# Optimization experiments

Measured on AMD Instinct MI355X. Metric: run time of the kernel, lower is better.

The kernel has to match this reference:

```python
import jax, jax.numpy as jnp
import numpy as np

SR = 44100
N_FFT = 2048
N_BINS = 64
HOP = 512
POWER = 2.0
FREQ_BINS = N_FFT // 2 + 1  # 1025
BATCH = 32
LEN_AUDIO = 441000  # 10 seconds at 44.1 kHz


def _fourier_kernels():
    # Periodic (fftbins=True) Hann window, matching scipy.signal.get_window('hann', n_fft)
    n = np.arange(N_FFT)
    window = 0.5 - 0.5 * np.cos(2.0 * np.pi * n / N_FFT)
    k = np.arange(FREQ_BINS)[:, None]  # [freq_bins, 1]
    phase = 2.0 * np.pi * k * n[None, :] / N_FFT  # [freq_bins, n_fft]
    wsin = (np.sin(phase) * window[None, :]).astype(np.float32)[:, None, :]  # [F,1,n_fft]
    wcos = (np.cos(phase) * window[None, :]).astype(np.float32)[:, None, :]
    return jnp.asarray(wsin), jnp.asarray(wcos)


def setup_inputs() -> dict:
    key = jax.random.key(0)
    k1, k2 = jax.random.split(key)
    x = jax.random.normal(k1, (BATCH, 1, LEN_AUDIO), dtype=jnp.float32)
    wsin, wcos = _fourier_kernels()
    # Gammatone filterbank matrix [n_bins, freq_bins]; treated as a fixed parameter.
    gammatone_basis = jax.random.uniform(k2, (N_BINS, FREQ_BINS), dtype=jnp.float32) * 0.01
    return {"x": x, "wsin": wsin, "wcos": wcos, "gammatone_basis": gammatone_basis}


def _conv1d(x, w, stride):
    # x: [B, 1, L], w: [F, 1, K] -> [B, F, T]
    return jax.lax.conv_general_dilated(
        x, w, window_strides=(stride,), padding='VALID',
        dimension_numbers=('NCH', 'OIH', 'NCH'))


def reference(x, wsin, wcos, gammatone_basis):
    pad = N_FFT // 2
    xp = jnp.pad(x, ((0, 0), (0, 0), (pad, pad)), mode='reflect')
    s = _conv1d(xp, wsin, HOP)
    c = _conv1d(xp, wcos, HOP)
    spec = jnp.sqrt(s * s + c * c) ** POWER  # [B, F, T]
    # [n_bins, F] @ [B, F, T] -> [B, n_bins, T]
    return jnp.einsum('nf,bft->bnt', gammatone_basis, spec)
```

## Files before the change

kernel.cpp:

```cpp
#include <hip/hip_runtime.h>
#include <stdint.h>

typedef __attribute__((ext_vector_type(4))) float f32x4;
typedef __attribute__((ext_vector_type(8))) short bf16x8;
typedef __attribute__((ext_vector_type(8))) unsigned short u16x8;
typedef __attribute__((ext_vector_type(2))) unsigned int u32x2;

#define B_SZ   32
#define L_AUD  441000
#define PAD_A  1024
#define LP     443048
#define T_FR   862
#define J_TOT  27584
#define JPAD   27648
#define F_BINS 1025
#define NFFT   2048
#define NB     64
#define FPAD   1152
#define NT_J   108
#define NT_F   9
#define NWG    (NT_J * NT_F)
#define ROWB   886096

#define W2_OFF     0
#define W2_BYTES   (NT_F * 32 * 16384)
#define GB2_OFF    W2_BYTES
#define GB2_BYTES  (NB * FPAD * 2)
#define UB_OFF     (GB2_OFF + GB2_BYTES)
#define UB_BYTES   ((size_t)JPAD * 2048 * 2)
#define WS_FOLD    (UB_OFF + UB_BYTES)
#define SLAB_BYTES ((size_t)NT_F * NB * JPAD * 4)
#define WS_FOLD_SLAB (WS_FOLD + SLAB_BYTES)

#define FB_XBP_OFF   0
#define FB_XBP_BYTES (B_SZ * LP * 2)
#define FB_WBT_OFF   FB_XBP_BYTES
#define FB_WBT_BYTES (NT_F * 32 * 2 * 16384)
#define FB_GB_OFF    (FB_WBT_OFF + FB_WBT_BYTES)
#define FB_WS_NEED   (FB_GB_OFF + GB2_BYTES)
#define FB_SLAB_OFF  FB_WS_NEED
#define FB_WS_BIG    ((size_t)FB_SLAB_OFF + SLAB_BYTES)

__device__ __forceinline__ uint16_t f2bf(float f) {
  union { float f; uint32_t u; } c; c.f = f;
  uint32_t r = c.u + 0x7FFFu + ((c.u >> 16) & 1u);
  return (uint16_t)(r >> 16);
}

__device__ __forceinline__ f32x4 mfma16(bf16x8 a, bf16x8 b, f32x4 c) {
  return __builtin_amdgcn_mfma_f32_16x16x32_bf16(a, b, c, 0, 0, 0);
}

#define GLD16(g, l) __builtin_amdgcn_global_load_lds( \
    (__attribute__((address_space(1))) void*)(g),     \
    (__attribute__((address_space(3))) void*)(l), 16, 0, 0)

__device__ __forceinline__ int refl(int p) {
  int s = p - PAD_A;
  s = s < 0 ? -s : s;
  s = s >= L_AUD ? (2 * L_AUD - 2 - s) : s;
  return s;
}


__global__ __launch_bounds__(256) void build_gb(const float* __restrict__ g,
                                                uint16_t* __restrict__ gb) {
  int i = blockIdx.x * 256 + threadIdx.x;
  int n = i / FPAD;
  int f = i - n * FPAD;
  gb[i] = f2bf(f < F_BINS ? g[n * F_BINS + f] : 0.0f);
}

__global__ __launch_bounds__(256) void reduce9(const float* __restrict__ slab,
                                               float* __restrict__ out) {
  int i = blockIdx.x * 256 + threadIdx.x;
  if (i >= J_TOT * NB) return;
  int b = i / (NB * T_FR);
  int rem = i - b * (NB * T_FR);
  int n = rem / T_FR;
  int t = rem - n * T_FR;
  int j = b * T_FR + t;
  float s = 0.f;
#pragma unroll
  for (int fb = 0; fb < NT_F; ++fb)
    s += slab[((size_t)fb * NB + n) * JPAD + j];
  out[i] = s;
}


__global__ __launch_bounds__(256) void build_wbt2(const float* __restrict__ wsin,
                                                  const float* __restrict__ wcos,
                                                  uint16_t* __restrict__ wbt) {
  int idx = blockIdx.x * 256 + threadIdx.x;
  int e = idx & 7;
  int s = (idx >> 3) & 7;
  int jp = (idx >> 6) & 127;
  int kkt = (idx >> 13) & 31;
  int fb = idx >> 18;
  int v = s ^ (jp & 7);
  int r = jp * 2 + (v >> 2);
  int k = (v & 3) * 8 + e;
  int plane = r >> 7;
  int f = fb * 128 + (r & 127);
  int m = kkt * 32 + k;
  float val = 0.f;
  if (f < F_BINS) {
    int mm = (m == 0) ? 1024 : m;
    val = plane ? wsin[(size_t)f * NFFT + mm] : wcos[(size_t)f * NFFT + mm];
  }
  wbt[idx] = f2bf(val);
}

__global__ __launch_bounds__(128) void build_ub(const float* __restrict__ x,
                                                uint16_t* __restrict__ ub) {
  __shared__ float xs[2048];
  int jg = blockIdx.x;
  int tid = threadIdx.x;
  uint16_t* outp = ub + (size_t)jg * 2048;
  if (jg >= J_TOT) {
    u16x8 z = (u16x8)0;
    *(u16x8*)(outp + tid * 8) = z;
    *(u16x8*)(outp + 1024 + tid * 8) = z;
    return;
  }
  int b = jg / T_FR, t = jg - b * T_FR;
  int c = t * 512;
  const float* xb = x + (size_t)b * L_AUD;
  if (t >= 2 && t <= 859) {
    const float4* src = (const float4*)(xb + c - PAD_A);
    float4* dl = (float4*)xs;
#pragma unroll
    for (int i = 0; i < 4; ++i) dl[tid * 4 + i] = src[tid * 4 + i];
  } else {
#pragma unroll
    for (int i = 0; i < 16; ++i) xs[tid * 16 + i] = xb[refl(c + tid * 16 + i)];
  }
  __syncthreads();
  int m0 = tid * 8;
  u16x8 vp, vm;
#pragma unroll
  for (int i = 0; i < 8; ++i) {
    int m = m0 + i;
    if (m == 0) { vp[i] = f2bf(xs[1024]); vm[i] = 0; }
    else {
      float a = xs[m], r = xs[2048 - m];
      vp[i] = f2bf(a + r);
      vm[i] = f2bf(a - r);
    }
  }
  *(u16x8*)(outp + m0) = vp;
  *(u16x8*)(outp + 1024 + m0) = vm;
}

template <bool USE_SLAB>
__global__ __launch_bounds__(512, 2) void gammatone_fold(
    const char* __restrict__ ub, const char* __restrict__ wbt2,
    const char* __restrict__ gb, float* __restrict__ dst) {
  __shared__ __align__(16) char smem[147456];

  const int tid = threadIdx.x;
  const int w = tid >> 6, l = tid & 63;
  const int lgrp = l >> 4, l15 = l & 15;
  const int fh = w >> 2, jq = w & 3;

  const int orig = blockIdx.x;
  const int xcd = orig & 7, slot = orig >> 3;
  const int q = NWG / 8, r = NWG & 7;
  const int wkid = (xcd < r ? xcd * (q + 1) : r * (q + 1) + (xcd - r) * q) + slot;
  const int jb = wkid / NT_F;
  const int fb = wkid - jb * NT_F;
  const int j0 = jb * 256;
  const int f0 = fb * 128;

  const int ssn = w >> 2, q4 = w & 3;
  const int aoff_sta = w * 2048 + l * 16;
  const int boff_sta = 16384 + ssn * 16384 + q4 * 4096 + l * 16;
  const int vsw = (l & 7) ^ (l >> 3);
  const char* bsrc[4];
#pragma unroll
  for (int i = 0; i < 4; ++i) {
    int col = j0 + q4 * 64 + i * 16 + (l >> 3) * 2 + (vsw >> 2);
    bsrc[i] = ub + (size_t)col * 4096 + ssn * 2048 + (vsw & 3) * 16;
  }
  const char* wbtA = wbt2 + (size_t)fb * 524288;

#define STAGEF(kkt, off) do {                                               \
    const char* ga_ = wbtA + (size_t)(kkt) * 16384 + aoff_sta;              \
    GLD16(ga_,        smem + (off) + aoff_sta);                             \
    GLD16(ga_ + 1024, smem + (off) + aoff_sta + 1024);                      \
    GLD16(bsrc[0] + (size_t)(kkt) * 64, smem + (off) + boff_sta);           \
    GLD16(bsrc[1] + (size_t)(kkt) * 64, smem + (off) + boff_sta + 1024);    \
    GLD16(bsrc[2] + (size_t)(kkt) * 64, smem + (off) + boff_sta + 2048);    \
    GLD16(bsrc[3] + (size_t)(kkt) * 64, smem + (off) + boff_sta + 3072);    \
  } while (0)

  const int slb = ((lgrp | ((l15 & 1) << 2)) ^ (l15 >> 1)) << 4;
  int aoff[8], bpo[4], bmo[4];
#pragma unroll
  for (int m = 0; m < 8; ++m)
    aoff[m] = ((m >> 2) * 64 + fh * 32 + (m & 3) * 8 + (l15 >> 1)) * 128 + slb;
#pragma unroll
  for (int n = 0; n < 4; ++n) {
    bpo[n] = 16384 + (jq * 32 + n * 8 + (l15 >> 1)) * 128 + slb;
    bmo[n] = bpo[n] + 16384;
  }

  STAGEF(0, 0);
  STAGEF(1, 49152);
  asm volatile("s_waitcnt vmcnt(6)" ::: "memory");
  asm volatile("s_barrier" ::: "memory");

  f32x4 acc[8][4];
#pragma unroll
  for (int m = 0; m < 8; ++m)
#pragma unroll
    for (int n = 0; n < 4; ++n) acc[m][n] = (f32x4){0.f, 0.f, 0.f, 0.f};

  unsigned b0 = 0, b1 = 49152, b2 = 98304;
  for (int kk = 0; kk < 32; ++kk) {
    bf16x8 av[8], bp[4], bm[4];
#pragma unroll
    for (int m = 0; m < 8; ++m) av[m] = *(const bf16x8*)(smem + b0 + aoff[m]);
#pragma unroll
    for (int n = 0; n < 4; ++n) {
      bp[n] = *(const bf16x8*)(smem + b0 + bpo[n]);
      bm[n] = *(const bf16x8*)(smem + b0 + bmo[n]);
    }
    if (kk < 30) STAGEF(kk + 2, b2);
    __builtin_amdgcn_s_setprio(1);
#pragma unroll
    for (int m = 0; m < 4; ++m)
#pragma unroll
      for (int n = 0; n < 4; ++n) {
        acc[m][n]     = mfma16(av[m],     bp[n], acc[m][n]);
        acc[m + 4][n] = mfma16(av[m + 4], bm[n], acc[m + 4][n]);
      }
    __builtin_amdgcn_s_setprio(0);
    if (kk < 30)       asm volatile("s_waitcnt vmcnt(6)" ::: "memory");
    else if (kk == 30) asm volatile("s_waitcnt vmcnt(0)" ::: "memory");
    asm volatile("s_barrier" ::: "memory");
    unsigned t = b0; b0 = b1; b1 = b2; b2 = t;
  }

#pragma unroll
  for (int m = 0; m < 4; ++m) {
    int fi = fh * 64 + m * 16 + lgrp * 4;
#pragma unroll
    for (int n = 0; n < 4; ++n) {
      int j = jq * 64 + n * 16 + l15;
      f32x4 c = acc[m][n], s = acc[m + 4][n];
      uint32_t lo = (uint32_t)f2bf(s.x * s.x + c.x * c.x) |
                    ((uint32_t)f2bf(s.y * s.y + c.y * c.y) << 16);
      uint32_t hi = (uint32_t)f2bf(s.z * s.z + c.z * c.z) |
                    ((uint32_t)f2bf(s.w * s.w + c.w * c.w) << 16);
      int off = j * 256 + ((fi * 2) ^ ((j & 7) << 4));
      *(u32x2*)(smem + off) = (u32x2){lo, hi};
    }
  }
  __syncthreads();

  f32x4 acc2[4][2];
#pragma unroll
  for (int m = 0; m < 4; ++m) {
    acc2[m][0] = (f32x4){0.f, 0.f, 0.f, 0.f};
    acc2[m][1] = (f32x4){0.f, 0.f, 0.f, 0.f};
  }
  const int jw = w * 32;
#pragma unroll
  for (int ks = 0; ks < 4; ++ks) {
    bf16x8 gf[4], sf[2];
#pragma unroll
    for (int m2 = 0; m2 < 4; ++m2) {
      int grow = m2 * 16 + l15;
      gf[m2] = *(const bf16x8*)(gb + ((size_t)grow * FPAD + f0 + ks * 32 + lgrp * 8) * 2);
    }
#pragma unroll
    for (int nf = 0; nf < 2; ++nf) {
      int j = jw + nf * 16 + l15;
      sf[nf] = *(const bf16x8*)(smem + j * 256 + (((ks * 32 + lgrp * 8) * 2) ^ ((j & 7) << 4)));
    }
#pragma unroll
    for (int m2 = 0; m2 < 4; ++m2)
#pragma unroll
      for (int nf = 0; nf < 2; ++nf)
        acc2[m2][nf] = mfma16(gf[m2], sf[nf], acc2[m2][nf]);
  }

#pragma unroll
  for (int nf = 0; nf < 2; ++nf) {
    int jg = j0 + jw + nf * 16 + l15;
    if (USE_SLAB) {
      float* sl = dst + ((size_t)fb * NB) * JPAD + jg;
#pragma unroll
      for (int m2 = 0; m2 < 4; ++m2)
#pragma unroll
        for (int r2 = 0; r2 < 4; ++r2) {
          int nout = m2 * 16 + lgrp * 4 + r2;
          sl[(size_t)nout * JPAD] = acc2[m2][nf][r2];
        }
    } else if (jg < J_TOT) {
      int b = jg / T_FR;
      int t = jg - b * T_FR;
      float* ob = dst + (size_t)(b * NB) * T_FR + t;
#pragma unroll
      for (int m2 = 0; m2 < 4; ++m2)
#pragma unroll
        for (int r2 = 0; r2 < 4; ++r2) {
          int nout = m2 * 16 + lgrp * 4 + r2;
          atomicAdd(ob + (size_t)nout * T_FR, acc2[m2][nf][r2]);
        }
    }
  }
}


__global__ __launch_bounds__(256) void build_xbp(const float* __restrict__ x,
                                                 uint16_t* __restrict__ xbp) {
  int i = blockIdx.x * 256 + threadIdx.x;
  int b = i / LP;
  int p = i - b * LP;
  xbp[i] = f2bf(x[b * L_AUD + refl(p)]);
}

__global__ __launch_bounds__(256) void build_wbtf(const float* __restrict__ wsin,
                                                  const float* __restrict__ wcos,
                                                  uint16_t* __restrict__ wbt) {
  int idx = blockIdx.x * 256 + threadIdx.x;
  int e = idx & 7;
  int l = (idx >> 3) & 63;
  int s = (idx >> 9) & 1;
  int fm = (idx >> 10) & 15;
  int kkt = (idx >> 14) & 31;
  int fb = idx >> 19;
  int tr = fm * 16 + (l & 15);
  int k = kkt * 64 + s * 32 + ((l >> 4) << 3) + e;
  int plane = (tr >> 6) & 1;
  int f = fb * 128 + ((tr >> 7) << 6) + (tr & 63);
  float v = (f < F_BINS) ? (plane ? wcos[f * NFFT + k] : wsin[f * NFFT + k]) : 0.0f;
  wbt[idx] = f2bf(v);
}

__device__ __forceinline__ void load_a2(bf16x8 (&d)[2][2], const char* p) {
  d[0][0] = *(const bf16x8*)(p);
  d[0][1] = *(const bf16x8*)(p + 1024);
  d[1][0] = *(const bf16x8*)(p + 2048);
  d[1][1] = *(const bf16x8*)(p + 3072);
}
__device__ __forceinline__ void load_b4(bf16x8 (&dst)[4][2], const char* p,
                                        int k0, int k1) {
#pragma unroll
  for (int n = 0; n < 4; ++n) {
    dst[n][0] = *(const bf16x8*)(p + n * 2048 + k0);
    dst[n][1] = *(const bf16x8*)(p + n * 2048 + k1);
  }
}
__device__ __forceinline__ void mfma_pair(f32x4 (*ac)[4],
                                          const bf16x8 (&av)[2][2],
                                          const bf16x8 (&bv)[4][2]) {
#pragma unroll
  for (int m = 0; m < 2; ++m)
#pragma unroll
    for (int n = 0; n < 4; ++n) {
      ac[m][n] = mfma16(av[m][0], bv[n][0], ac[m][n]);
      ac[m][n] = mfma16(av[m][1], bv[n][1], ac[m][n]);
    }
}

template <bool USE_SLAB>
__global__ __launch_bounds__(512, 2) void gammatone_fb(
    const char* __restrict__ xbp, const char* __restrict__ wbt,
    const char* __restrict__ gb, float* __restrict__ dst) {
  __shared__ __align__(16) char smem[65536];

  const int tid = threadIdx.x;
  const int w = tid >> 6, l = tid & 63;
  const int lgrp = l >> 4, l15 = l & 15;
  const int wr = w >> 2, wc = w & 3;

  const int orig = blockIdx.y * NT_J + blockIdx.x;
  const int xcd = orig & 7, slot = orig >> 3;
  const int q = NWG / 8, r = NWG & 7;
  const int wkid = (xcd < r ? xcd * (q + 1) : r * (q + 1) + (xcd - r) * q) + slot;
  const int fb = wkid / NT_J;
  const int jb = wkid - fb * NT_J;
  const int j0 = jb * 256;
  const int f0 = fb * 128;

  const int xr = (((tid & 7) << 4)) ^ ((((tid >> 3) & 7)) << 4);
  size_t fbase[2][2];
#pragma unroll
  for (int h = 0; h < 2; ++h)
#pragma unroll
    for (int i = 0; i < 2; ++i) {
      int col = j0 + h * 128 + i * 64 + (tid >> 3);
      if (col > J_TOT - 1) col = J_TOT - 1;
      int b = col / T_FR;
      int t = col - b * T_FR;
      fbase[h][i] = (size_t)b * ROWB + (size_t)t * 1024 + (size_t)xr;
    }

#define STAGE_B2(kkt, buf) do {                                             \
    char* d0_ = smem + (buf) * 32768;                                       \
    char* d1_ = smem + (buf) * 32768 + 16384;                               \
    GLD16(xbp + fbase[0][0] + (size_t)(kkt) * 128, d0_ + w * 1024 + l * 16);\
    GLD16(xbp + fbase[0][1] + (size_t)(kkt) * 128, d0_ + 8192 + w * 1024 + l * 16);\
    GLD16(xbp + fbase[1][0] + (size_t)(kkt) * 128, d1_ + w * 1024 + l * 16);\
    GLD16(xbp + fbase[1][1] + (size_t)(kkt) * 128, d1_ + 8192 + w * 1024 + l * 16);\
  } while (0)

  const int albase = l15 * 128;
  const int xa = (l15 & 7) << 4;
  const int k0 = (lgrp * 16) ^ xa;
  const int k1 = (64 + lgrp * 16) ^ xa;
  const int jrb = (wc & 1) * 64;
  const char* Bb0 = smem + (wc >> 1) * 16384 + jrb * 128 + albase;
  const char* Bb1 = Bb0 + 32768;
  const char* wbt_a = wbt + (size_t)fb * 32 * 32768 + wr * 16384 + (size_t)l * 16;

  STAGE_B2(0, 0);
  STAGE_B2(1, 1);
  asm volatile("s_waitcnt vmcnt(0)" ::: "memory");
  __builtin_amdgcn_s_barrier();

  f32x4 acc[8][4];
#pragma unroll
  for (int m = 0; m < 8; ++m)
#pragma unroll
    for (int n = 0; n < 4; ++n) acc[m][n] = (f32x4){0.f, 0.f, 0.f, 0.f};

  bf16x8 bvA[4][2], bvB[4][2], av0[2][2], av1[2][2];
  load_b4(bvA, Bb0, k0, k1);
  load_a2(av0, wbt_a);
  asm volatile("s_waitcnt lgkmcnt(0)" ::: "memory");
  __builtin_amdgcn_s_barrier();

#define SP1 __builtin_amdgcn_s_setprio(1)
#define SP0 __builtin_amdgcn_s_setprio(0)

#define TILEFB(KK, bvC, bvN, BbN, STG, NXT) do {                            \
    const char* aT = wbt_a + (size_t)(KK) * 32768;                          \
    if (STG) STAGE_B2((KK) + 2, (KK) & 1);                                  \
    load_a2(av1, aT + 2 * 2048);                                            \
    SP1; mfma_pair(&acc[0], av0, bvC); SP0;                                 \
    load_a2(av0, aT + 4 * 2048);                                            \
    SP1; mfma_pair(&acc[2], av1, bvC); SP0;                                 \
    load_a2(av1, aT + 6 * 2048);                                            \
    if (NXT) load_b4(bvN, BbN, k0, k1);                                     \
    SP1; mfma_pair(&acc[4], av0, bvC); SP0;                                 \
    if (NXT) load_a2(av0, wbt_a + (size_t)((KK) + 1) * 32768);              \
    SP1; mfma_pair(&acc[6], av1, bvC); SP0;                                 \
    asm volatile("s_waitcnt lgkmcnt(0)" ::: "memory");                      \
    __builtin_amdgcn_s_barrier();                                           \
  } while (0)

  for (int kk = 0; kk < 30; kk += 2) {
    TILEFB(kk,     bvA, bvB, Bb1, 1, 1);
    TILEFB(kk + 1, bvB, bvA, Bb0, 1, 1);
  }
  TILEFB(30, bvA, bvB, Bb1, 0, 1);
  TILEFB(31, bvB, bvA, Bb0, 0, 0);

  __syncthreads();
#pragma unroll
  for (int m = 0; m < 4; ++m) {
    int fi = wr * 64 + m * 16 + lgrp * 4;
#pragma unroll
    for (int n = 0; n < 4; ++n) {
      int j = wc * 64 + n * 16 + l15;
      f32x4 s = acc[m][n], c = acc[m + 4][n];
      uint32_t lo = (uint32_t)f2bf(s.x * s.x + c.x * c.x) |
                    ((uint32_t)f2bf(s.y * s.y + c.y * c.y) << 16);
      uint32_t hi = (uint32_t)f2bf(s.z * s.z + c.z * c.z) |
                    ((uint32_t)f2bf(s.w * s.w + c.w * c.w) << 16);
      int off = j * 256 + ((fi * 2) ^ ((j & 7) << 4));
      *(u32x2*)(smem + off) = (u32x2){lo, hi};
    }
  }
  __syncthreads();

  f32x4 acc2[4][2];
#pragma unroll
  for (int m = 0; m < 4; ++m) {
    acc2[m][0] = (f32x4){0.f, 0.f, 0.f, 0.f};
    acc2[m][1] = (f32x4){0.f, 0.f, 0.f, 0.f};
  }
  const int jw = w * 32;
#pragma unroll
  for (int ks = 0; ks < 4; ++ks) {
    bf16x8 gf[4], sf[2];
#pragma unroll
    for (int m2 = 0; m2 < 4; ++m2) {
      int grow = m2 * 16 + l15;
      gf[m2] = *(const bf16x8*)(gb + ((size_t)grow * FPAD + f0 + ks * 32 + lgrp * 8) * 2);
    }
#pragma unroll
    for (int nf = 0; nf < 2; ++nf) {
      int j = jw + nf * 16 + l15;
      sf[nf] = *(const bf16x8*)(smem + j * 256 + (((ks * 32 + lgrp * 8) * 2) ^ ((j & 7) << 4)));
    }
#pragma unroll
    for (int m2 = 0; m2 < 4; ++m2)
#pragma unroll
      for (int nf = 0; nf < 2; ++nf)
        acc2[m2][nf] = mfma16(gf[m2], sf[nf], acc2[m2][nf]);
  }

#pragma unroll
  for (int nf = 0; nf < 2; ++nf) {
    int jg = j0 + jw + nf * 16 + l15;
    if (USE_SLAB) {
      float* sl = dst + ((size_t)fb * NB) * JPAD + jg;
#pragma unroll
      for (int m2 = 0; m2 < 4; ++m2)
#pragma unroll
        for (int r2 = 0; r2 < 4; ++r2) {
          int nout = m2 * 16 + lgrp * 4 + r2;
          sl[(size_t)nout * JPAD] = acc2[m2][nf][r2];
        }
    } else if (jg < J_TOT) {
      int b = jg / T_FR;
      int t = jg - b * T_FR;
      float* ob = dst + (size_t)(b * NB) * T_FR + t;
#pragma unroll
      for (int m2 = 0; m2 < 4; ++m2)
#pragma unroll
        for (int r2 = 0; r2 < 4; ++r2) {
          int nout = m2 * 16 + lgrp * 4 + r2;
          atomicAdd(ob + (size_t)nout * T_FR, acc2[m2][nf][r2]);
        }
    }
  }
}

extern "C" void kernel_launch(void* const* d_in, const int* in_sizes, int n_in,
                              void* d_out, int out_size, void* d_ws, size_t ws_size,
                              hipStream_t stream) {
  (void)in_sizes; (void)n_in;
  const float* x    = (const float*)d_in[0];
  const float* wsin = (const float*)d_in[1];
  const float* wcos = (const float*)d_in[2];
  const float* g    = (const float*)d_in[3];
  char* ws = (char*)d_ws;

  if (ws_size >= (size_t)WS_FOLD) {
    uint16_t* wbt2 = (uint16_t*)(ws + W2_OFF);
    uint16_t* gbp  = (uint16_t*)(ws + GB2_OFF);
    uint16_t* ub   = (uint16_t*)(ws + UB_OFF);
    build_wbt2<<<(W2_BYTES / 2) / 256, 256, 0, stream>>>(wsin, wcos, wbt2);
    build_gb<<<(NB * FPAD) / 256, 256, 0, stream>>>(g, gbp);
    build_ub<<<JPAD, 128, 0, stream>>>(x, ub);
    if (ws_size >= (size_t)WS_FOLD_SLAB) {
      float* slab = (float*)(ws + WS_FOLD);
      gammatone_fold<true><<<NWG, 512, 0, stream>>>(
          (const char*)ub, (const char*)wbt2, (const char*)gbp, slab);
      reduce9<<<(J_TOT * NB + 255) / 256, 256, 0, stream>>>(slab, (float*)d_out);
    } else {
      hipMemsetAsync(d_out, 0, (size_t)out_size * sizeof(float), stream);
      gammatone_fold<false><<<NWG, 512, 0, stream>>>(
          (const char*)ub, (const char*)wbt2, (const char*)gbp, (float*)d_out);
    }
    return;
  }

  if (ws_size < (size_t)FB_WS_NEED) return;
  uint16_t* xbp = (uint16_t*)(ws + FB_XBP_OFF);
  uint16_t* wbt = (uint16_t*)(ws + FB_WBT_OFF);
  uint16_t* gbp = (uint16_t*)(ws + FB_GB_OFF);
  build_xbp<<<(B_SZ * LP) / 256, 256, 0, stream>>>(x, xbp);
  build_wbtf<<<(FB_WBT_BYTES / 2) / 256, 256, 0, stream>>>(wsin, wcos, wbt);
  build_gb<<<(NB * FPAD) / 256, 256, 0, stream>>>(g, gbp);
  if (ws_size >= (size_t)FB_WS_BIG) {
    float* slab = (float*)(ws + FB_SLAB_OFF);
    gammatone_fb<true><<<dim3(NT_J, NT_F), 512, 0, stream>>>(
        (const char*)xbp, (const char*)wbt, (const char*)gbp, slab);
    reduce9<<<(J_TOT * NB + 255) / 256, 256, 0, stream>>>(slab, (float*)d_out);
  } else {
    hipMemsetAsync(d_out, 0, (size_t)out_size * sizeof(float), stream);
    gammatone_fb<false><<<dim3(NT_J, NT_F), 512, 0, stream>>>(
        (const char*)xbp, (const char*)wbt, (const char*)gbp, (float*)d_out);
  }
}
```

Baseline: 215.8 us.

## Replace triple-buffered LDS pipeline with single buffer and register prefetch

Cuts the LDS allocation of the gammatone_fold kernel from three 48KB stage buffers to one 64KB region. The next k-tile is loaded into that same buffer while the MFMAs run on fragments already held in registers. The aim is to lower LDS pressure so that two workgroups can fit per CU, as the launch bounds request. The cost is that global-load latency is now hidden by only one stage, and there are two barriers per iteration plus a full vmcnt(0) wait.

```diff
diff --git a/kernel.cpp b/kernel.cpp
--- a/kernel.cpp
+++ b/kernel.cpp
@@ -156,7 +156,7 @@
 __global__ __launch_bounds__(512, 2) void gammatone_fold(
     const char* __restrict__ ub, const char* __restrict__ wbt2,
     const char* __restrict__ gb, float* __restrict__ dst) {
-  __shared__ __align__(16) char smem[147456];
+  __shared__ __align__(16) char smem[65536];
 
   const int tid = threadIdx.x;
   const int w = tid >> 6, l = tid & 63;
@@ -184,14 +184,14 @@
   }
   const char* wbtA = wbt2 + (size_t)fb * 524288;
 
-#define STAGEF(kkt, off) do {                                               \
+#define STAGEF(kkt) do {                                                    \
     const char* ga_ = wbtA + (size_t)(kkt) * 16384 + aoff_sta;              \
-    GLD16(ga_,        smem + (off) + aoff_sta);                             \
-    GLD16(ga_ + 1024, smem + (off) + aoff_sta + 1024);                      \
-    GLD16(bsrc[0] + (size_t)(kkt) * 64, smem + (off) + boff_sta);           \
-    GLD16(bsrc[1] + (size_t)(kkt) * 64, smem + (off) + boff_sta + 1024);    \
-    GLD16(bsrc[2] + (size_t)(kkt) * 64, smem + (off) + boff_sta + 2048);    \
-    GLD16(bsrc[3] + (size_t)(kkt) * 64, smem + (off) + boff_sta + 3072);    \
+    GLD16(ga_,        smem + aoff_sta);                                     \
+    GLD16(ga_ + 1024, smem + aoff_sta + 1024);                              \
+    GLD16(bsrc[0] + (size_t)(kkt) * 64, smem + boff_sta);                   \
+    GLD16(bsrc[1] + (size_t)(kkt) * 64, smem + boff_sta + 1024);            \
+    GLD16(bsrc[2] + (size_t)(kkt) * 64, smem + boff_sta + 2048);            \
+    GLD16(bsrc[3] + (size_t)(kkt) * 64, smem + boff_sta + 3072);            \
   } while (0)
 
   const int slb = ((lgrp | ((l15 & 1) << 2)) ^ (l15 >> 1)) << 4;
@@ -205,9 +205,8 @@
     bmo[n] = bpo[n] + 16384;
   }
 
-  STAGEF(0, 0);
-  STAGEF(1, 49152);
-  asm volatile("s_waitcnt vmcnt(6)" ::: "memory");
+  STAGEF(0);
+  asm volatile("s_waitcnt vmcnt(0)" ::: "memory");
   asm volatile("s_barrier" ::: "memory");
 
   f32x4 acc[8][4];
@@ -216,17 +215,19 @@
 #pragma unroll
     for (int n = 0; n < 4; ++n) acc[m][n] = (f32x4){0.f, 0.f, 0.f, 0.f};
 
-  unsigned b0 = 0, b1 = 49152, b2 = 98304;
+  bf16x8 av[8], bp[4], bm[4];
+#pragma unroll
+  for (int m = 0; m < 8; ++m) av[m] = *(const bf16x8*)(smem + aoff[m]);
+#pragma unroll
+  for (int n = 0; n < 4; ++n) {
+    bp[n] = *(const bf16x8*)(smem + bpo[n]);
+    bm[n] = *(const bf16x8*)(smem + bmo[n]);
+  }
+
   for (int kk = 0; kk < 32; ++kk) {
-    bf16x8 av[8], bp[4], bm[4];
-#pragma unroll
-    for (int m = 0; m < 8; ++m) av[m] = *(const bf16x8*)(smem + b0 + aoff[m]);
-#pragma unroll
-    for (int n = 0; n < 4; ++n) {
-      bp[n] = *(const bf16x8*)(smem + b0 + bpo[n]);
-      bm[n] = *(const bf16x8*)(smem + b0 + bmo[n]);
-    }
-    if (kk < 30) STAGEF(kk + 2, b2);
+    asm volatile("s_waitcnt lgkmcnt(0)" ::: "memory");
+    asm volatile("s_barrier" ::: "memory");
+    if (kk < 31) STAGEF(kk + 1);
     __builtin_amdgcn_s_setprio(1);
 #pragma unroll
     for (int m = 0; m < 4; ++m)
@@ -236,12 +237,20 @@
         acc[m + 4][n] = mfma16(av[m + 4], bm[n], acc[m + 4][n]);
       }
     __builtin_amdgcn_s_setprio(0);
-    if (kk < 30)       asm volatile("s_waitcnt vmcnt(6)" ::: "memory");
-    else if (kk == 30) asm volatile("s_waitcnt vmcnt(0)" ::: "memory");
-    asm volatile("s_barrier" ::: "memory");
-    unsigned t = b0; b0 = b1; b1 = b2; b2 = t;
-  }
-
+    if (kk < 31) {
+      asm volatile("s_waitcnt vmcnt(0)" ::: "memory");
+      asm volatile("s_barrier" ::: "memory");
+#pragma unroll
+      for (int m = 0; m < 8; ++m) av[m] = *(const bf16x8*)(smem + aoff[m]);
+#pragma unroll
+      for (int n = 0; n < 4; ++n) {
+        bp[n] = *(const bf16x8*)(smem + bpo[n]);
+        bm[n] = *(const bf16x8*)(smem + bmo[n]);
+      }
+    }
+  }
+
+  __syncthreads();
 #pragma unroll
   for (int m = 0; m < 4; ++m) {
     int fi = fh * 64 + m * 16 + lgrp * 4;
```

Result: slower. 251.9 us (+16.7%).

## Split warps by sin/cos plane and combine power spectrum via LDS

Applied to the files above, without the earlier changes.

Reassigns the eight waves in the fused STFT+gammatone kernel so each wave computes only one plane (cos or sin) over a 64-row by 128-column tile. Previously each wave held both planes for a smaller column range. The new mapping reads 12 bf16x8 fragments per k-step instead of 16 for the same 32 MFMAs, which cuts LDS read traffic in the main loop. The cost is that the power |s|²+|c|² must now be combined across waves through shared memory. That adds a barrier, a read-modify-write pass, and an extra bf16 rounding of the intermediate cos² term.

```diff
diff --git a/kernel.cpp b/kernel.cpp
--- a/kernel.cpp
+++ b/kernel.cpp
@@ -45,6 +45,9 @@
   union { float f; uint32_t u; } c; c.f = f;
   uint32_t r = c.u + 0x7FFFu + ((c.u >> 16) & 1u);
   return (uint16_t)(r >> 16);
+}
+__device__ __forceinline__ float bf2f(uint32_t u) {
+  union { uint32_t u; float f; } c; c.u = u << 16; return c.f;
 }
 
 __device__ __forceinline__ f32x4 mfma16(bf16x8 a, bf16x8 b, f32x4 c) {
@@ -161,7 +164,9 @@
   const int tid = threadIdx.x;
   const int w = tid >> 6, l = tid & 63;
   const int lgrp = l >> 4, l15 = l & 15;
-  const int fh = w >> 2, jq = w & 3;
+  const int plane = w >> 2;
+  const int rw = (w >> 1) & 1;
+  const int jw = w & 1;
 
   const int orig = blockIdx.x;
   const int xcd = orig & 7, slot = orig >> 3;
@@ -195,46 +200,39 @@
   } while (0)
 
   const int slb = ((lgrp | ((l15 & 1) << 2)) ^ (l15 >> 1)) << 4;
-  int aoff[8], bpo[4], bmo[4];
-#pragma unroll
-  for (int m = 0; m < 8; ++m)
-    aoff[m] = ((m >> 2) * 64 + fh * 32 + (m & 3) * 8 + (l15 >> 1)) * 128 + slb;
-#pragma unroll
-  for (int n = 0; n < 4; ++n) {
-    bpo[n] = 16384 + (jq * 32 + n * 8 + (l15 >> 1)) * 128 + slb;
-    bmo[n] = bpo[n] + 16384;
-  }
+  int aoff[4], bvo[8];
+#pragma unroll
+  for (int m = 0; m < 4; ++m)
+    aoff[m] = (plane * 64 + rw * 32 + m * 8 + (l15 >> 1)) * 128 + slb;
+#pragma unroll
+  for (int n = 0; n < 8; ++n)
+    bvo[n] = 16384 + plane * 16384 + (jw * 64 + n * 8 + (l15 >> 1)) * 128 + slb;
 
   STAGEF(0, 0);
   STAGEF(1, 49152);
   asm volatile("s_waitcnt vmcnt(6)" ::: "memory");
   asm volatile("s_barrier" ::: "memory");
 
-  f32x4 acc[8][4];
-#pragma unroll
-  for (int m = 0; m < 8; ++m)
-#pragma unroll
-    for (int n = 0; n < 4; ++n) acc[m][n] = (f32x4){0.f, 0.f, 0.f, 0.f};
+  f32x4 acc[4][8];
+#pragma unroll
+  for (int m = 0; m < 4; ++m)
+#pragma unroll
+    for (int n = 0; n < 8; ++n) acc[m][n] = (f32x4){0.f, 0.f, 0.f, 0.f};
 
   unsigned b0 = 0, b1 = 49152, b2 = 98304;
   for (int kk = 0; kk < 32; ++kk) {
-    bf16x8 av[8], bp[4], bm[4];
-#pragma unroll
-    for (int m = 0; m < 8; ++m) av[m] = *(const bf16x8*)(smem + b0 + aoff[m]);
-#pragma unroll
-    for (int n = 0; n < 4; ++n) {
-      bp[n] = *(const bf16x8*)(smem + b0 + bpo[n]);
-      bm[n] = *(const bf16x8*)(smem + b0 + bmo[n]);
-    }
+    bf16x8 av[4], bv[8];
+#pragma unroll
+    for (int m = 0; m < 4; ++m) av[m] = *(const bf16x8*)(smem + b0 + aoff[m]);
+#pragma unroll
+    for (int n = 0; n < 8; ++n) bv[n] = *(const bf16x8*)(smem + b0 + bvo[n]);
     if (kk < 30) STAGEF(kk + 2, b2);
     __builtin_amdgcn_s_setprio(1);
 #pragma unroll
     for (int m = 0; m < 4; ++m)
 #pragma unroll
-      for (int n = 0; n < 4; ++n) {
-        acc[m][n]     = mfma16(av[m],     bp[n], acc[m][n]);
-        acc[m + 4][n] = mfma16(av[m + 4], bm[n], acc[m + 4][n]);
-      }
+      for (int n = 0; n < 8; ++n)
+        acc[m][n] = mfma16(av[m], bv[n], acc[m][n]);
     __builtin_amdgcn_s_setprio(0);
     if (kk < 30)       asm volatile("s_waitcnt vmcnt(6)" ::: "memory");
     else if (kk == 30) asm volatile("s_waitcnt vmcnt(0)" ::: "memory");
@@ -242,19 +240,41 @@
     unsigned t = b0; b0 = b1; b1 = b2; b2 = t;
   }
 
-#pragma unroll
-  for (int m = 0; m < 4; ++m) {
-    int fi = fh * 64 + m * 16 + lgrp * 4;
-#pragma unroll
-    for (int n = 0; n < 4; ++n) {
-      int j = jq * 64 + n * 16 + l15;
-      f32x4 c = acc[m][n], s = acc[m + 4][n];
-      uint32_t lo = (uint32_t)f2bf(s.x * s.x + c.x * c.x) |
-                    ((uint32_t)f2bf(s.y * s.y + c.y * c.y) << 16);
-      uint32_t hi = (uint32_t)f2bf(s.z * s.z + c.z * c.z) |
-                    ((uint32_t)f2bf(s.w * s.w + c.w * c.w) << 16);
-      int off = j * 256 + ((fi * 2) ^ ((j & 7) << 4));
-      *(u32x2*)(smem + off) = (u32x2){lo, hi};
+  __syncthreads();
+  if (plane == 0) {
+#pragma unroll
+    for (int m = 0; m < 4; ++m) {
+      int fi = rw * 64 + m * 16 + lgrp * 4;
+#pragma unroll
+      for (int n = 0; n < 8; ++n) {
+        int j = jw * 128 + n * 16 + l15;
+        f32x4 c = acc[m][n];
+        uint32_t lo = (uint32_t)f2bf(c.x * c.x) |
+                      ((uint32_t)f2bf(c.y * c.y) << 16);
+        uint32_t hi = (uint32_t)f2bf(c.z * c.z) |
+                      ((uint32_t)f2bf(c.w * c.w) << 16);
+        int off = j * 256 + ((fi * 2) ^ ((j & 7) << 4));
+        *(u32x2*)(smem + off) = (u32x2){lo, hi};
+      }
+    }
+  }
+  __syncthreads();
+  if (plane == 1) {
+#pragma unroll
+    for (int m = 0; m < 4; ++m) {
+      int fi = rw * 64 + m * 16 + lgrp * 4;
+#pragma unroll
+      for (int n = 0; n < 8; ++n) {
+        int j = jw * 128 + n * 16 + l15;
+        int off = j * 256 + ((fi * 2) ^ ((j & 7) << 4));
+        u32x2 v = *(u32x2*)(smem + off);
+        f32x4 s = acc[m][n];
+        uint32_t lo = (uint32_t)f2bf(bf2f(v.x & 0xffffu) + s.x * s.x) |
+                      ((uint32_t)f2bf(bf2f(v.x >> 16) + s.y * s.y) << 16);
+        uint32_t hi = (uint32_t)f2bf(bf2f(v.y & 0xffffu) + s.z * s.z) |
+                      ((uint32_t)f2bf(bf2f(v.y >> 16) + s.w * s.w) << 16);
+        *(u32x2*)(smem + off) = (u32x2){lo, hi};
+      }
     }
   }
   __syncthreads();
@@ -265,7 +285,7 @@
     acc2[m][0] = (f32x4){0.f, 0.f, 0.f, 0.f};
     acc2[m][1] = (f32x4){0.f, 0.f, 0.f, 0.f};
   }
-  const int jw = w * 32;
+  const int jwq = w * 32;
 #pragma unroll
   for (int ks = 0; ks < 4; ++ks) {
     bf16x8 gf[4], sf[2];
@@ -276,7 +296,7 @@
     }
 #pragma unroll
     for (int nf = 0; nf < 2; ++nf) {
-      int j = jw + nf * 16 + l15;
+      int j = jwq + nf * 16 + l15;
       sf[nf] = *(const bf16x8*)(smem + j * 256 + (((ks * 32 + lgrp * 8) * 2) ^ ((j & 7) << 4)));
     }
 #pragma unroll
@@ -288,7 +308,7 @@
 
 #pragma unroll
   for (int nf = 0; nf < 2; ++nf) {
-    int jg = j0 + jw + nf * 16 + l15;
+    int jg = j0 + jwq + nf * 16 + l15;
     if (USE_SLAB) {
       float* sl = dst + ((size_t)fb * NB) * JPAD + jg;
 #pragma unroll
```

New measurement: 218.4 us. Within noise of the previous version (+1.2%).
